# Performance work log

Hardware: AMD Instinct MI355X
Metric: run time of the kernel (lower is better)

The kernel has to match this reference:

```python
import math
import jax, jax.numpy as jnp
import numpy as np

D = 128
R = 64
BETA = 1.0


def setup_inputs() -> dict:
    key = jax.random.key(0)
    k1, k2 = jax.random.split(key)
    X_tilde = jax.random.normal(k1, (8, 2048, D), dtype=jnp.float32)
    W = jax.random.normal(k2, (D, R), dtype=jnp.float32) / math.sqrt(R)
    return {"X_tilde": X_tilde, "W": W}


def reference(X_tilde, W):
    # S = W W^T / sqrt(d*r), shape (d, d)
    d, r = W.shape
    S = (W @ W.T) / math.sqrt(d * r)
    B, T, _ = X_tilde.shape
    # gram = X S X^T, shape (B, T, T)
    XS = jnp.einsum('btd,de->bte', X_tilde, S)
    gram = jnp.einsum('bte,bse->bts', XS, X_tilde)
    # trace-centering: subtract (tr(gram)/T) * I
    trace = jnp.einsum('btt->b', gram)  # (B,)
    eye = jnp.eye(T, dtype=X_tilde.dtype)
    centered = gram - (trace / T)[:, None, None] * eye[None, :, :]
    scores = centered / math.sqrt(d)  # normalize_sqrt_d=True
    A = jax.nn.softmax(BETA * scores, axis=-1)  # (B, T, T)
    Y_hat = jnp.einsum('bts,bsd->btd', A, X_tilde)
    return Y_hat
```

## Files before the change

### kernel.cpp

```cpp
#include <hip/hip_runtime.h>
#include <hip/hip_bf16.h>
#include <math.h>

#define D_DIM 128
#define R_DIM 64
#define T_DIM 2048
#define B_DIM 8
#define NS 4
#define SCHUNK (T_DIM / NS)
#define SBLK 64
#define NIT (SCHUNK / SBLK)
#define KE_CONST (0.08838834764831845f * 1.4426950408889634f)

typedef __attribute__((ext_vector_type(8))) short bf16x8;
typedef __attribute__((ext_vector_type(4))) short s16x4;
typedef __attribute__((ext_vector_type(4))) float f32x4;
typedef __attribute__((ext_vector_type(16))) float f32x16;

__device__ inline unsigned short f2bf(float f) {
  union { float f; unsigned int u; } v; v.f = f;
  return (unsigned short)((v.u + 0x7FFFu + ((v.u >> 16) & 1u)) >> 16);
}
__device__ inline float bf2f(unsigned short u) {
  union { unsigned int u; float f; } v; v.u = ((unsigned int)u) << 16;
  return v.f;
}
__device__ inline unsigned int cvt_pk_bf16(float lo, float hi) {
  unsigned int r;
  asm("v_cvt_pk_bf16_f32 %0, %1, %2" : "=v"(r) : "v"(lo), "v"(hi));
  return r;
}
__device__ inline void permswap(unsigned int& a, unsigned int& b) {
  asm("v_permlane32_swap_b32 %0, %1" : "+v"(a), "+v"(b));
}
__device__ inline float fexp2(float x) {
  float r;
  asm("v_exp_f32 %0, %1" : "=v"(r) : "v"(x));
  return r;
}

__device__ inline void async16(const short* l, const unsigned short* g) {
  __builtin_amdgcn_global_load_lds(
      (const __attribute__((address_space(1))) unsigned int*)g,
      (__attribute__((address_space(3))) unsigned int*)l, 16, 0, 0);
}

__global__ void k_s(const float* __restrict__ W, unsigned short* __restrict__ Sb) {
  int gid = blockIdx.x * 256 + threadIdx.x;
  int i = gid >> 7, j = gid & 127;
  const float* wi = W + i * R_DIM;
  const float* wj = W + j * R_DIM;
  float acc = 0.f;
#pragma unroll 8
  for (int r = 0; r < R_DIM; ++r) acc += wi[r] * wj[r];
  int off = (((i >> 4) * 4 + (j >> 5)) * 64 + ((j & 31) >> 3) * 16 + (i & 15)) * 8 + (j & 7);
  Sb[off] = f2bf(acc * 0.011048543456039806f);
}

__global__ void __launch_bounds__(128) k_prep(
    const float* __restrict__ X, const unsigned short* __restrict__ Sb,
    unsigned short* __restrict__ Qb, unsigned short* __restrict__ Xb,
    unsigned short* __restrict__ Xt, float* __restrict__ part) {
  const int tid = threadIdx.x;
  const int w = tid >> 6, lane = tid & 63;
  const int g = lane >> 4, c = lane & 15;
  const int b = blockIdx.y;
  const int t0 = blockIdx.x * 32;
  const int tw = t0 + w * 16;

  __shared__ __align__(16) short xbT[D_DIM * 32];
  __shared__ float red[2];

  union FU { unsigned int wd[4]; bf16x8 v; };
  bf16x8 xf[4];
#pragma unroll
  for (int kc = 0; kc < 4; ++kc) {
    const float* xp = X + ((size_t)(b * T_DIM + tw + c)) * D_DIM + kc * 32 + g * 8;
    f32x4 a = *(const f32x4*)xp;
    f32x4 bb = *(const f32x4*)(xp + 4);
    FU f;
    f.wd[0] = cvt_pk_bf16(a[0], a[1]);
    f.wd[1] = cvt_pk_bf16(a[2], a[3]);
    f.wd[2] = cvt_pk_bf16(bb[0], bb[1]);
    f.wd[3] = cvt_pk_bf16(bb[2], bb[3]);
    xf[kc] = f.v;
    *(bf16x8*)(Xb + ((size_t)(b * T_DIM + tw + c)) * D_DIM + kc * 32 + g * 8) = f.v;
#pragma unroll
    for (int jw = 0; jw < 4; ++jw) {
      unsigned int wv = f.wd[jw];
      int e = kc * 32 + g * 8 + jw * 2;
      xbT[(e + 0) * 32 + w * 16 + c] = (short)wv;
      xbT[(e + 1) * 32 + w * 16 + c] = (short)(wv >> 16);
    }
  }

  f32x4 acc[8];
#pragma unroll
  for (int dc = 0; dc < 8; ++dc) acc[dc] = (f32x4){0.f, 0.f, 0.f, 0.f};
#pragma unroll
  for (int dc = 0; dc < 8; ++dc) {
    bf16x8 sf[4];
#pragma unroll
    for (int kc = 0; kc < 4; ++kc)
      sf[kc] = *(const bf16x8*)(Sb + ((size_t)(dc * 4 + kc) * 64 + lane) * 8);
#pragma unroll
    for (int kc = 0; kc < 4; ++kc)
      acc[dc] = __builtin_amdgcn_mfma_f32_16x16x32_bf16(xf[kc], sf[kc], acc[dc], 0, 0, 0);
  }

  __syncthreads();

  float trp = 0.f;
#pragma unroll
  for (int dc = 0; dc < 8; ++dc)
#pragma unroll
    for (int r = 0; r < 4; ++r) {
      float q = acc[dc][r];
      float x = bf2f((unsigned short)xbT[(dc * 16 + c) * 32 + w * 16 + g * 4 + r]);
      trp += q * x;
      int t = tw + g * 4 + r;
      size_t qoff = (((size_t)(b * 64 + (t >> 5)) * 8 + dc) * 512 +
                     ((c >> 3) * 32 + (t & 31)) * 8 + (c & 7));
      Qb[qoff] = (unsigned short)cvt_pk_bf16(q * KE_CONST, 0.f);
    }

#pragma unroll
  for (int p = 0; p < 4; ++p) {
    int row = p * 32 + (tid >> 2);
    bf16x8 v = *(const bf16x8*)&xbT[row * 32 + (tid & 3) * 8];
    *(bf16x8*)(Xt + ((size_t)(b * D_DIM + row)) * T_DIM + t0 + (tid & 3) * 8) = v;
  }

  trp += __shfl_xor(trp, 1); trp += __shfl_xor(trp, 2);
  trp += __shfl_xor(trp, 4); trp += __shfl_xor(trp, 8);
  trp += __shfl_xor(trp, 16); trp += __shfl_xor(trp, 32);
  if (lane == 0) red[w] = trp;
  __syncthreads();
  if (tid == 0) part[b * 64 + blockIdx.x] = red[0] + red[1];
}

__global__ void __launch_bounds__(256, 2) k_attn(
    const unsigned short* __restrict__ Qb, const unsigned short* __restrict__ Xb,
    const unsigned short* __restrict__ Xt, const float* __restrict__ part,
    unsigned short* __restrict__ accp, float* __restrict__ rsp) {
  const int tid = threadIdx.x;
  const int wave = tid >> 6, lane = tid & 63;
  const int tl = lane & 31;
  const int h = lane >> 5;
  const int lin = blockIdx.x;
  const int b = lin & 7;
  const int kk = lin >> 3;
  const int ns = kk & 3;
  const int tile = kk >> 2;
  const int t0w = tile * 128 + wave * 32;

  const unsigned short* Xbb = Xb + (size_t)b * T_DIM * D_DIM;
  const unsigned short* Xtb = Xt + (size_t)b * D_DIM * T_DIM;

  float tv = part[b * 64 + lane];
  tv += __shfl_xor(tv, 1); tv += __shfl_xor(tv, 2);
  tv += __shfl_xor(tv, 4); tv += __shfl_xor(tv, 8);
  tv += __shfl_xor(tv, 16); tv += __shfl_xor(tv, 32);
  const float ctrK = tv * (1.0f / T_DIM) * KE_CONST;
  const float expCtr = fexp2(-ctrK);

  __shared__ __align__(16) short sKs[2][SBLK * D_DIM];
  __shared__ __align__(16) short sVs[2][D_DIM * SBLK];

  int oK[8];
#pragma unroll
  for (int kc = 0; kc < 8; ++kc)
    oK[kc] = tl * 128 + (((kc * 2 + h) ^ (tl & 15)) * 8);

  const unsigned short* qbase =
      Qb + ((size_t)(b * 64 + tile * 4 + wave)) * 8 * 512;
  bf16x8 qf[8];
#pragma unroll
  for (int kc = 0; kc < 8; ++kc)
    qf[kc] = *(const bf16x8*)(qbase + (size_t)kc * 512 + lane * 8);

  f32x16 acc[4];
#pragma unroll
  for (int dt = 0; dt < 4; ++dt)
#pragma unroll
    for (int r = 0; r < 16; ++r) acc[dt][r] = 0.f;
  float denacc = 0.f;

  const int s_beg = ns * SCHUNK;

  auto stage = [&](int buf, int sb) {
#pragma unroll
    for (int q = 0; q < 4; ++q) {
      int j = wave * 256 + q * 64 + lane;
      int row = j >> 4, sc = j & 15;
      int lc = sc ^ (row & 15);
      async16(&sKs[buf][(wave * 256 + q * 64) * 8],
              Xbb + (size_t)(sb + row) * D_DIM + lc * 8);
    }
#pragma unroll
    for (int q = 0; q < 4; ++q) {
      int j = wave * 256 + q * 64 + lane;
      int row = j >> 3, sc = j & 7;
      int lc = sc ^ (row & 7);
      async16(&sVs[buf][(wave * 256 + q * 64) * 8],
              Xtb + (size_t)row * T_DIM + sb + lc * 8);
    }
  };

  stage(0, s_beg);

  for (int it = 0; it < NIT; ++it) {
    const int buf = it & 1;
    const int sb = s_beg + it * SBLK;

    if (it < NIT - 1) {
      stage(buf ^ 1, sb + SBLK);
      asm volatile("s_waitcnt vmcnt(8)" ::: "memory");
    } else {
      asm volatile("s_waitcnt vmcnt(0)" ::: "memory");
    }
    __builtin_amdgcn_sched_barrier(0);
    __builtin_amdgcn_s_barrier();

    const short* kb = &sKs[buf][0];
    const short* vb = &sVs[buf][0];

#pragma unroll
    for (int sub = 0; sub < 2; ++sub) {
      bf16x8 kf[8];
#pragma unroll
      for (int kc = 0; kc < 8; ++kc)
        kf[kc] = *(const bf16x8*)(kb + sub * 32 * 128 + oK[kc]);
      bf16x8 vf[4][2];
#pragma unroll
      for (int dt = 0; dt < 4; ++dt)
#pragma unroll
        for (int sck = 0; sck < 2; ++sck)
          vf[dt][sck] = *(const bf16x8*)(vb + (dt * 32 + tl) * 64 +
                                         (((sub * 4 + sck * 2 + h) ^ (tl & 7)) * 8));

      f32x16 sa, sb2;
#pragma unroll
      for (int r = 0; r < 16; ++r) { sa[r] = 0.f; sb2[r] = 0.f; }
#pragma unroll
      for (int kc = 0; kc < 4; ++kc) {
        sa  = __builtin_amdgcn_mfma_f32_32x32x16_bf16(kf[kc],     qf[kc],     sa,  0, 0, 0);
        sb2 = __builtin_amdgcn_mfma_f32_32x32x16_bf16(kf[kc + 4], qf[kc + 4], sb2, 0, 0, 0);
      }
      f32x16 sc = sa + sb2;

      const bool isd = (sb + sub * 32 == t0w);

#pragma unroll
      for (int sck = 0; sck < 2; ++sck) {
        float p[8];
#pragma unroll
        for (int q = 0; q < 8; ++q) p[q] = fexp2(sc[sck * 8 + q]);
        if (isd) {
#pragma unroll
          for (int q = 0; q < 8; ++q) {
            int rowid = (q & 3) + 8 * (q >> 2) + 16 * sck + 4 * h;
            if (rowid == tl) p[q] *= expCtr;
          }
        }
#pragma unroll
        for (int q = 0; q < 8; ++q) denacc += p[q];
        unsigned int W0 = cvt_pk_bf16(p[0], p[1]);
        unsigned int W1 = cvt_pk_bf16(p[2], p[3]);
        unsigned int W2 = cvt_pk_bf16(p[4], p[5]);
        unsigned int W3 = cvt_pk_bf16(p[6], p[7]);
        permswap(W0, W2);
        permswap(W1, W3);
        union PU { unsigned int wd[4]; bf16x8 v; } pu;
        pu.wd[0] = W0; pu.wd[1] = W1; pu.wd[2] = W2; pu.wd[3] = W3;
#pragma unroll
        for (int dt = 0; dt < 4; ++dt)
          acc[dt] = __builtin_amdgcn_mfma_f32_32x32x16_bf16(pu.v, vf[dt][sck],
                                                            acc[dt], 0, 0, 0);
      }
    }

    __builtin_amdgcn_s_barrier();
  }

  float den = denacc + __shfl_xor(denacc, 32);
  if (lane < 32)
    rsp[(b * NS + ns) * T_DIM + t0w + lane] = den;

  const size_t pbase = ((size_t)(b * NS + ns)) * T_DIM * D_DIM;
#pragma unroll
  for (int dt = 0; dt < 4; ++dt)
#pragma unroll
    for (int r = 0; r < 16; ++r) {
      int rowid = (r & 3) + 8 * (r >> 2) + 4 * h;
      accp[pbase + (size_t)(t0w + rowid) * D_DIM + dt * 32 + tl] =
          (unsigned short)cvt_pk_bf16(acc[dt][r], 0.f);
    }
}

__global__ void __launch_bounds__(256) k_comb(
    const unsigned short* __restrict__ accp, const float* __restrict__ rsp,
    float* __restrict__ out) {
  const int lin = blockIdx.x;
  const int b = lin & 7;
  const int kk = lin >> 3;
  int ib = kk * 2048 + threadIdx.x * 8;
  int d = ib & 127;
  int t = ib >> 7;
  float num[8] = {0.f, 0.f, 0.f, 0.f, 0.f, 0.f, 0.f, 0.f};
  float den = 0.f;
#pragma unroll
  for (int ns = 0; ns < NS; ++ns) {
    const unsigned short* p =
        accp + (((size_t)(b * NS + ns)) * T_DIM + t) * D_DIM + d;
    bf16x8 v = *(const bf16x8*)p;
#pragma unroll
    for (int j = 0; j < 8; ++j) num[j] += bf2f((unsigned short)v[j]);
    den += rsp[(b * NS + ns) * T_DIM + t];
  }
  float inv = 1.0f / den;
  float* o = out + ((size_t)b * T_DIM * D_DIM + ib);
  f32x4 o0 = (f32x4){num[0] * inv, num[1] * inv, num[2] * inv, num[3] * inv};
  f32x4 o1 = (f32x4){num[4] * inv, num[5] * inv, num[6] * inv, num[7] * inv};
  *(f32x4*)(o + 0) = o0;
  *(f32x4*)(o + 4) = o1;
}

extern "C" void kernel_launch(void* const* d_in, const int* in_sizes, int n_in,
                              void* d_out, int out_size, void* d_ws, size_t ws_size,
                              hipStream_t stream) {
  const float* X = (const float*)d_in[0];
  const float* W = (const float*)d_in[1];
  float* out = (float*)d_out;
  char* ws = (char*)d_ws;

  unsigned short* Sb = (unsigned short*)(ws);
  float* part        = (float*)(ws + 32768);
  unsigned short* Qb = (unsigned short*)(ws + 65536);
  unsigned short* Xb = (unsigned short*)(ws + 65536 + 4194304);
  unsigned short* Xt = (unsigned short*)(ws + 65536 + 2 * 4194304);
  unsigned short* accp = (unsigned short*)(ws + 65536 + 3 * 4194304);
  float* rsp         = (float*)(ws + 65536 + 3 * 4194304 + 16777216);

  k_s<<<64, 256, 0, stream>>>(W, Sb);
  k_prep<<<dim3(T_DIM / 32, B_DIM), 128, 0, stream>>>(X, Sb, Qb, Xb, Xt, part);
  k_attn<<<(T_DIM / 128) * NS * B_DIM, 256, 0, stream>>>(Qb, Xb, Xt, part, accp, rsp);
  k_comb<<<B_DIM * 128, 256, 0, stream>>>(accp, rsp, out);
}
```

Baseline: 43.74 us.

## Split k_prep reduction dimension across waves to double block count

k_prep now handles 16 tokens per block instead of 32, and its two waves split the 128-wide D reduction (two K-chunks each) rather than taking separate token groups. Wave 1's partial MFMA accumulators go through shared memory to wave 0, which adds them, writes Qb and computes the trace partial. The trace partial array grows to 128 entries per batch, and k_attn sums both halves. This doubles the grid for better GPU fill in the prep stage, at the cost of an LDS exchange and wave 1 sitting idle during the epilogue.

```diff
diff --git a/kernel.cpp b/kernel.cpp
--- a/kernel.cpp
+++ b/kernel.cpp
@@ -65,17 +65,17 @@
   const int w = tid >> 6, lane = tid & 63;
   const int g = lane >> 4, c = lane & 15;
   const int b = blockIdx.y;
-  const int t0 = blockIdx.x * 32;
-  const int tw = t0 + w * 16;
-
-  __shared__ __align__(16) short xbT[D_DIM * 32];
-  __shared__ float red[2];
+  const int t0 = blockIdx.x * 16;
+
+  __shared__ __align__(16) short xbT[D_DIM * 16];
+  __shared__ __align__(16) float accLds[8 * 64 * 4];
 
   union FU { unsigned int wd[4]; bf16x8 v; };
-  bf16x8 xf[4];
-#pragma unroll
-  for (int kc = 0; kc < 4; ++kc) {
-    const float* xp = X + ((size_t)(b * T_DIM + tw + c)) * D_DIM + kc * 32 + g * 8;
+  bf16x8 xf[2];
+#pragma unroll
+  for (int kcl = 0; kcl < 2; ++kcl) {
+    const int kc = w * 2 + kcl;
+    const float* xp = X + ((size_t)(b * T_DIM + t0 + c)) * D_DIM + kc * 32 + g * 8;
     f32x4 a = *(const f32x4*)xp;
     f32x4 bb = *(const f32x4*)(xp + 4);
     FU f;
@@ -83,14 +83,14 @@
     f.wd[1] = cvt_pk_bf16(a[2], a[3]);
     f.wd[2] = cvt_pk_bf16(bb[0], bb[1]);
     f.wd[3] = cvt_pk_bf16(bb[2], bb[3]);
-    xf[kc] = f.v;
-    *(bf16x8*)(Xb + ((size_t)(b * T_DIM + tw + c)) * D_DIM + kc * 32 + g * 8) = f.v;
+    xf[kcl] = f.v;
+    *(bf16x8*)(Xb + ((size_t)(b * T_DIM + t0 + c)) * D_DIM + kc * 32 + g * 8) = f.v;
 #pragma unroll
     for (int jw = 0; jw < 4; ++jw) {
       unsigned int wv = f.wd[jw];
       int e = kc * 32 + g * 8 + jw * 2;
-      xbT[(e + 0) * 32 + w * 16 + c] = (short)wv;
-      xbT[(e + 1) * 32 + w * 16 + c] = (short)(wv >> 16);
+      xbT[(e + 0) * 16 + c] = (short)wv;
+      xbT[(e + 1) * 16 + c] = (short)(wv >> 16);
     }
   }
 
@@ -99,44 +99,50 @@
   for (int dc = 0; dc < 8; ++dc) acc[dc] = (f32x4){0.f, 0.f, 0.f, 0.f};
 #pragma unroll
   for (int dc = 0; dc < 8; ++dc) {
-    bf16x8 sf[4];
-#pragma unroll
-    for (int kc = 0; kc < 4; ++kc)
-      sf[kc] = *(const bf16x8*)(Sb + ((size_t)(dc * 4 + kc) * 64 + lane) * 8);
-#pragma unroll
-    for (int kc = 0; kc < 4; ++kc)
-      acc[dc] = __builtin_amdgcn_mfma_f32_16x16x32_bf16(xf[kc], sf[kc], acc[dc], 0, 0, 0);
-  }
-
+    bf16x8 sf[2];
+#pragma unroll
+    for (int kcl = 0; kcl < 2; ++kcl)
+      sf[kcl] = *(const bf16x8*)(Sb + ((size_t)(dc * 4 + w * 2 + kcl) * 64 + lane) * 8);
+#pragma unroll
+    for (int kcl = 0; kcl < 2; ++kcl)
+      acc[dc] = __builtin_amdgcn_mfma_f32_16x16x32_bf16(xf[kcl], sf[kcl], acc[dc], 0, 0, 0);
+  }
+
+  if (w == 1) {
+#pragma unroll
+    for (int dc = 0; dc < 8; ++dc)
+#pragma unroll
+      for (int r = 0; r < 4; ++r)
+        accLds[dc * 256 + lane * 4 + r] = acc[dc][r];
+  }
   __syncthreads();
 
-  float trp = 0.f;
-#pragma unroll
-  for (int dc = 0; dc < 8; ++dc)
-#pragma unroll
-    for (int r = 0; r < 4; ++r) {
-      float q = acc[dc][r];
-      float x = bf2f((unsigned short)xbT[(dc * 16 + c) * 32 + w * 16 + g * 4 + r]);
-      trp += q * x;
-      int t = tw + g * 4 + r;
-      size_t qoff = (((size_t)(b * 64 + (t >> 5)) * 8 + dc) * 512 +
-                     ((c >> 3) * 32 + (t & 31)) * 8 + (c & 7));
-      Qb[qoff] = (unsigned short)cvt_pk_bf16(q * KE_CONST, 0.f);
-    }
-
-#pragma unroll
-  for (int p = 0; p < 4; ++p) {
-    int row = p * 32 + (tid >> 2);
-    bf16x8 v = *(const bf16x8*)&xbT[row * 32 + (tid & 3) * 8];
-    *(bf16x8*)(Xt + ((size_t)(b * D_DIM + row)) * T_DIM + t0 + (tid & 3) * 8) = v;
-  }
-
-  trp += __shfl_xor(trp, 1); trp += __shfl_xor(trp, 2);
-  trp += __shfl_xor(trp, 4); trp += __shfl_xor(trp, 8);
-  trp += __shfl_xor(trp, 16); trp += __shfl_xor(trp, 32);
-  if (lane == 0) red[w] = trp;
-  __syncthreads();
-  if (tid == 0) part[b * 64 + blockIdx.x] = red[0] + red[1];
+  if (w == 0) {
+    float trp = 0.f;
+#pragma unroll
+    for (int dc = 0; dc < 8; ++dc)
+#pragma unroll
+      for (int r = 0; r < 4; ++r) {
+        float q = acc[dc][r] + accLds[dc * 256 + lane * 4 + r];
+        float x = bf2f((unsigned short)xbT[(dc * 16 + c) * 16 + g * 4 + r]);
+        trp += q * x;
+        int t = t0 + g * 4 + r;
+        size_t qoff = (((size_t)(b * 64 + (t >> 5)) * 8 + dc) * 512 +
+                       ((c >> 3) * 32 + (t & 31)) * 8 + (c & 7));
+        Qb[qoff] = (unsigned short)cvt_pk_bf16(q * KE_CONST, 0.f);
+      }
+    trp += __shfl_xor(trp, 1); trp += __shfl_xor(trp, 2);
+    trp += __shfl_xor(trp, 4); trp += __shfl_xor(trp, 8);
+    trp += __shfl_xor(trp, 16); trp += __shfl_xor(trp, 32);
+    if (lane == 0) part[b * 128 + blockIdx.x] = trp;
+  }
+
+#pragma unroll
+  for (int p = 0; p < 2; ++p) {
+    int row = p * 64 + (tid >> 1);
+    bf16x8 v = *(const bf16x8*)&xbT[row * 16 + (tid & 1) * 8];
+    *(bf16x8*)(Xt + ((size_t)(b * D_DIM + row)) * T_DIM + t0 + (tid & 1) * 8) = v;
+  }
 }
 
 __global__ void __launch_bounds__(256, 2) k_attn(
@@ -157,7 +163,7 @@
   const unsigned short* Xbb = Xb + (size_t)b * T_DIM * D_DIM;
   const unsigned short* Xtb = Xt + (size_t)b * D_DIM * T_DIM;
 
-  float tv = part[b * 64 + lane];
+  float tv = part[b * 128 + lane] + part[b * 128 + 64 + lane];
   tv += __shfl_xor(tv, 1); tv += __shfl_xor(tv, 2);
   tv += __shfl_xor(tv, 4); tv += __shfl_xor(tv, 8);
   tv += __shfl_xor(tv, 16); tv += __shfl_xor(tv, 32);
@@ -343,7 +349,7 @@
   float* rsp         = (float*)(ws + 65536 + 3 * 4194304 + 16777216);
 
   k_s<<<64, 256, 0, stream>>>(W, Sb);
-  k_prep<<<dim3(T_DIM / 32, B_DIM), 128, 0, stream>>>(X, Sb, Qb, Xb, Xt, part);
+  k_prep<<<dim3(T_DIM / 16, B_DIM), 128, 0, stream>>>(X, Sb, Qb, Xb, Xt, part);
   k_attn<<<(T_DIM / 128) * NS * B_DIM, 256, 0, stream>>>(Qb, Xb, Xt, part, accp, rsp);
   k_comb<<<B_DIM * 128, 256, 0, stream>>>(accp, rsp, out);
 }
```

Measured after the change: 43.60 us, median of 3. No clear change (-0.3%).
